# Performance work log

Measured on AMD Instinct MI355X. Metric: run time of the kernel, lower is better.

Reference implementation:

```python
import jax, jax.numpy as jnp
import numpy as np

WIN = 16
HEADS = 4


def _window_partition(x, win):
    B, H, W, C = x.shape
    x = x.reshape(B, H // win, win, W // win, win, C)
    x = x.transpose(0, 1, 3, 2, 4, 5)
    return x.reshape(-1, win * win, C)


def _reverse_window_partition(x, win, H, W):
    N, _, C = x.shape
    x = x.reshape(-1, H // win, W // win, win, win, C)
    x = x.transpose(0, 1, 3, 2, 4, 5)
    return x.reshape(-1, H, W, C)


def setup_inputs() -> dict:
    key = jax.random.key(0)
    ks = jax.random.split(key, 7)
    B, H, W, C = 2, 256, 256, 96
    s = 0.02
    return {
        "x": jax.random.normal(ks[0], (B, H, W, C), jnp.float32),
        "qkv_w": jax.random.normal(ks[1], (C, 3 * C), jnp.float32) * s,
        "qkv_b": jax.random.normal(ks[2], (3 * C,), jnp.float32) * s,
        "pe_w": jax.random.normal(ks[3], (3, 3, 1, C), jnp.float32) * s,  # depthwise HWIO
        "pe_b": jax.random.normal(ks[4], (C,), jnp.float32) * s,
        "out_w": jax.random.normal(ks[5], (C, C), jnp.float32) * s,
        "out_b": jax.random.normal(ks[6], (C,), jnp.float32) * s,
    }


def reference(x, qkv_w, qkv_b, pe_w, pe_b, out_w, out_b):
    B, H, W, C = x.shape
    win, heads = WIN, HEADS
    hd = C // heads

    z = _window_partition(x, win)
    N, S, _ = z.shape

    qkv = z @ qkv_w + qkv_b                       # (N, S, 3C)
    # headify then chunk(3): each head's 3*hd channels split into q,k,v
    qkv = qkv.reshape(N, S, heads, 3, hd).transpose(0, 2, 3, 1, 4)  # (N, h, 3, S, hd)
    q, k, v = qkv[:, :, 0], qkv[:, :, 1], qkv[:, :, 2]

    # Locally-enhanced PE: depthwise 3x3 conv on de-headified v
    v_img = v.transpose(0, 2, 1, 3).reshape(N, win, win, C)  # NHWC
    lepe = jax.lax.conv_general_dilated(
        v_img, pe_w, (1, 1), 'SAME',
        dimension_numbers=('NHWC', 'HWIO', 'NHWC'),
        feature_group_count=C) + pe_b
    lepe = lepe.reshape(N, S, heads, hd).transpose(0, 2, 1, 3)  # (N, h, S, hd)

    # per-window SDPA (default scale 1/sqrt(hd))
    scale = 1.0 / jnp.sqrt(jnp.asarray(hd, x.dtype))
    attn = jax.nn.softmax(jnp.einsum('nhsd,nhtd->nhst', q, k) * scale, axis=-1)
    o = jnp.einsum('nhst,nhtd->nhsd', attn, v) + lepe

    o = o.transpose(0, 2, 1, 3).reshape(N, S, C)
    o = _reverse_window_partition(o, win, H, W)   # (B, H, W, C)
    return o @ out_w + out_b
```

## Files before the change

kernel.cpp:

```cpp
#include <hip/hip_runtime.h>


typedef __attribute__((ext_vector_type(8))) short bf16x8;
typedef __attribute__((ext_vector_type(4))) float f32x4;

#define MFMA(a, b, c) __builtin_amdgcn_mfma_f32_16x16x32_bf16(a, b, c, 0, 0, 0)

#if __has_builtin(__builtin_amdgcn_exp2f)
#define EXP2F(x) __builtin_amdgcn_exp2f(x)
#else
#define EXP2F(x) exp2f(x)
#endif

#define SCALE2 (0.20412414523193154f * 1.4426950408889634f)

#define OFF_WT   0u
#define OFF_B2   55296u
#define OFF_WTO  56448u
#define OFF_OB   75904u

__device__ __forceinline__ unsigned short f2bf(float f) {
    union { float f; unsigned int u; } v; v.f = f;
    unsigned int u = v.u;
    return (unsigned short)((u + 0x7FFFu + ((u >> 16) & 1u)) >> 16);
}
__device__ __forceinline__ float bf2f(unsigned short h) {
    union { unsigned int u; float f; } v; v.u = ((unsigned int)h) << 16;
    return v.f;
}
__device__ __forceinline__ unsigned int pk2bf(float a, float b) {
#if __has_builtin(__builtin_amdgcn_cvt_pk_bf16_f32)
    auto p = __builtin_amdgcn_cvt_pk_bf16_f32(a, b);
    union { decltype(p) v; unsigned int u; } cv; cv.v = p;
    return cv.u;
#else
    return (unsigned int)f2bf(a) | ((unsigned int)f2bf(b) << 16);
#endif
}
__device__ __forceinline__ float frcp(float x) {
#if __has_builtin(__builtin_amdgcn_rcpf)
    return __builtin_amdgcn_rcpf(x);
#else
    return 1.0f / x;
#endif
}

__global__ void prep_kernel(const float* __restrict__ qkv_w,
                            const float* __restrict__ qkv_b,
                            const float* __restrict__ out_w,
                            unsigned short* __restrict__ wt,
                            float* __restrict__ b2,
                            unsigned short* __restrict__ wto) {
    const int stride = gridDim.x * 256;
    int i0 = blockIdx.x * 256 + threadIdx.x;
    for (int i = i0; i < 288 * 96; i += stride) {
        const int c = i / 96, k = i % 96;
        float v = qkv_w[k * 288 + c];
        if ((c % 72) < 24) v *= SCALE2;
        wt[i] = f2bf(v);
    }
    for (int i = i0; i < 288; i += stride) {
        float v = qkv_b[i];
        if ((i % 72) < 24) v *= SCALE2;
        b2[i] = v;
    }
    for (int i = i0; i < 96 * 96; i += stride) {
        const int c = i / 96, k = i % 96;
        wto[i] = f2bf(out_w[k * 96 + c]);
    }
}

__global__ __launch_bounds__(512) __attribute__((amdgpu_waves_per_eu(4, 4)))
void fused_kernel(const float* __restrict__ x,
                  const unsigned short* __restrict__ wt,
                  const float* __restrict__ b2,
                  const float* __restrict__ pe_w,
                  const float* __restrict__ pe_b,
                  unsigned short* __restrict__ Ob) {
    __shared__ unsigned short sK[256 * 24 + 8];
    __shared__ unsigned short sVT[32 * 264];
    __shared__ unsigned short sPO[8 * 32 * 40];
    __shared__ float sPW[216];
    __shared__ float sPB[24];

    const int n = blockIdx.x, tid = threadIdx.x;
    const int w = tid >> 6, l = tid & 63;
    const int lm = l & 15, lq = l >> 4;
    const int bW = n >> 8, hy = (n >> 4) & 15, wx = n & 15;
    unsigned short* Pw = &sPO[w * 32 * 40];

    if (tid < 64) {
        ushort4 ones; ones.x = ones.y = ones.z = ones.w = (unsigned short)0x3F80;
        *(ushort4*)&sVT[24 * 264 + tid * 4] = ones;
    }

    bf16x8 zf[2][3];
#pragma unroll
    for (int t4 = 0; t4 < 2; t4++) {
        const int y = w * 2 + t4;
        const size_t grow = (size_t)((bW * 256 + hy * 16 + y) * 256 + wx * 16 + lm);
        const float* xr = x + grow * 96 + lq * 8;
#pragma unroll
        for (int ks = 0; ks < 3; ks++) {
            const float4 p0 = *(const float4*)(xr + ks * 32);
            const float4 p1 = *(const float4*)(xr + ks * 32 + 4);
            union { unsigned int u[4]; bf16x8 v; } cv;
            cv.u[0] = pk2bf(p0.x, p0.y); cv.u[1] = pk2bf(p0.z, p0.w);
            cv.u[2] = pk2bf(p1.x, p1.y); cv.u[3] = pk2bf(p1.z, p1.w);
            zf[t4][ks] = cv.v;
        }
    }

    for (int h = 0; h < 4; h++) {
        __syncthreads();

#pragma unroll
        for (int mt = 0; mt < 3; mt++) {
            bf16x8 af[3];
#pragma unroll
            for (int ks = 0; ks < 3; ks++)
                af[ks] = *(const bf16x8*)(wt + (h * 72 + mt * 16 + lm) * 96 + ks * 32 + lq * 8);
            const int r48 = mt * 16 + lq * 4;
            const float4 bias = *(const float4*)(b2 + h * 72 + r48);
#pragma unroll
            for (int t4 = 0; t4 < 2; t4++) {
                f32x4 acc = {0.f, 0.f, 0.f, 0.f};
#pragma unroll
                for (int ks = 0; ks < 3; ks++) acc = MFMA(af[ks], zf[t4][ks], acc);
                uint2 pk;
                pk.x = pk2bf(acc[0] + bias.x, acc[1] + bias.y);
                pk.y = pk2bf(acc[2] + bias.z, acc[3] + bias.w);
                const int tl = t4 * 16 + lm;
                if (r48 < 24) *(uint2*)&Pw[tl * 40 + r48] = pk;
                else          *(uint2*)&sK[(w * 32 + tl) * 24 + (r48 - 24)] = pk;
            }
        }

#pragma unroll
        for (int nv = 0; nv < 2; nv++) {
            const int ch = nv * 16 + lm;
            const int vrow = h * 72 + 48 + (ch < 24 ? ch : 23);
            bf16x8 bw[3];
#pragma unroll
            for (int ks = 0; ks < 3; ks++)
                bw[ks] = *(const bf16x8*)(wt + vrow * 96 + ks * 32 + lq * 8);
            const float bv = b2[vrow];
#pragma unroll
            for (int t4 = 0; t4 < 2; t4++) {
                f32x4 acc = {0.f, 0.f, 0.f, 0.f};
#pragma unroll
                for (int ks = 0; ks < 3; ks++) acc = MFMA(zf[t4][ks], bw[ks], acc);
                if (ch < 24) {
                    uint2 pk;
                    pk.x = pk2bf(acc[0] + bv, acc[1] + bv);
                    pk.y = pk2bf(acc[2] + bv, acc[3] + bv);
                    *(uint2*)&sVT[ch * 264 + w * 32 + t4 * 16 + lq * 4] = pk;
                }
            }
        }

        for (int i = tid; i < 216; i += 512) sPW[i] = pe_w[(i / 24) * 96 + h * 24 + (i % 24)];
        if (tid < 24) sPB[tid] = pe_b[h * 24 + tid];

        __syncthreads();

        bf16x8 qf[2];
#pragma unroll
        for (int b = 0; b < 2; b++) {
            bf16x8 qv = *(const bf16x8*)&Pw[(b * 16 + lm) * 40 + lq * 8];
            if (lq == 3) qv = (bf16x8)(short)0;
            qf[b] = qv;
        }

        f32x4 oa[2][2];
#pragma unroll
        for (int b = 0; b < 2; b++)
#pragma unroll
            for (int c = 0; c < 2; c++) oa[b][c] = (f32x4){0.f, 0.f, 0.f, 0.f};

        for (int kc = 0; kc < 8; kc++) {
            bf16x8 kfc[2];
#pragma unroll
            for (int a = 0; a < 2; a++)
                kfc[a] = *(const bf16x8*)&sK[(kc * 32 + a * 16 + lm) * 24 + lq * 8];
#pragma unroll
            for (int a = 0; a < 2; a++) {
                f32x4 s[2];
#pragma unroll
                for (int b = 0; b < 2; b++)
                    s[b] = MFMA(kfc[a], qf[b], ((f32x4){0.f, 0.f, 0.f, 0.f}));
#pragma unroll
                for (int b = 0; b < 2; b++) {
                    uint2 pk;
                    pk.x = pk2bf(EXP2F(s[b][0]), EXP2F(s[b][1]));
                    pk.y = pk2bf(EXP2F(s[b][2]), EXP2F(s[b][3]));
                    *(uint2*)&Pw[(b * 16 + lm) * 40 + a * 16 + lq * 4] = pk;
                }
            }
            bf16x8 vb[2];
#pragma unroll
            for (int c = 0; c < 2; c++)
                vb[c] = *(const bf16x8*)&sVT[(c * 16 + lm) * 264 + kc * 32 + lq * 8];
#pragma unroll
            for (int b = 0; b < 2; b++) {
                const bf16x8 pa = *(const bf16x8*)&Pw[(b * 16 + lm) * 40 + lq * 8];
#pragma unroll
                for (int c = 0; c < 2; c++) oa[b][c] = MFMA(pa, vb[c], oa[b][c]);
            }
        }

        float w9[2][9], pb2[2];
#pragma unroll
        for (int c = 0; c < 2; c++) {
            const int ch = c * 16 + lm;
            if (ch < 24) {
#pragma unroll
                for (int ta = 0; ta < 9; ta++) w9[c][ta] = sPW[ta * 24 + ch];
                pb2[c] = sPB[ch];
            }
        }
#pragma unroll
        for (int b = 0; b < 2; b++) {
            float rinv[4];
#pragma unroll
            for (int r = 0; r < 4; r++)
                rinv[r] = frcp(__shfl(oa[b][1][r], (l & 48) | 8, 64));
            const int y = w * 2 + b;
            const int x0 = lq * 4;
#pragma unroll
            for (int c = 0; c < 2; c++) {
                const int ch = c * 16 + lm;
                if (ch < 24) {
                    float lep[4] = {pb2[c], pb2[c], pb2[c], pb2[c]};
                    const unsigned short* vbase = &sVT[ch * 264];
#pragma unroll
                    for (int dy = -1; dy <= 1; dy++) {
                        const int ny = y + dy;
                        if ((unsigned)ny > 15u) continue;
                        const unsigned short* vrow = vbase + ny * 16;
                        const float wl = w9[c][(dy + 1) * 3 + 0];
                        const float wm = w9[c][(dy + 1) * 3 + 1];
                        const float wr = w9[c][(dy + 1) * 3 + 2];
#pragma unroll
                        for (int d = -1; d <= 4; d++) {
                            const int xx = x0 + d;
                            if ((unsigned)xx > 15u) continue;
                            const float v = bf2f(vrow[xx]);
                            if (d - 1 >= 0 && d - 1 <= 3) lep[d - 1] = fmaf(v, wr, lep[d - 1]);
                            if (d >= 0 && d <= 3)         lep[d]     = fmaf(v, wm, lep[d]);
                            if (d + 1 <= 3)               lep[d + 1] = fmaf(v, wl, lep[d + 1]);
                        }
                    }
#pragma unroll
                    for (int r = 0; r < 4; r++) {
                        const float val = oa[b][c][r] * rinv[r] + lep[r];
                        const size_t gtok = (size_t)n * 256 + w * 32 + b * 16 + lq * 4 + r;
                        Ob[gtok * 96 + h * 24 + ch] = f2bf(val);
                    }
                }
            }
        }
    }
}

__global__ __launch_bounds__(256) __attribute__((amdgpu_waves_per_eu(4, 4)))
void oproj_kernel(const unsigned short* __restrict__ Ob,
                  const unsigned short* __restrict__ wto,
                  const float* __restrict__ out_b,
                  float* __restrict__ out) {
    const int chunk = blockIdx.x, tid = threadIdx.x;
    const int w = tid >> 6, l = tid & 63;
    const int lm = l & 15, lq = l >> 4;
    const int n = chunk >> 1;
    const int T0 = (chunk & 1) << 7;
    const int bW = n >> 8, hy = (n >> 4) & 15, wx = n & 15;
    const int tb = T0 + w * 32;
    const size_t gb = (size_t)n * 256 + tb;

    bf16x8 aO[2][3];
#pragma unroll
    for (int b = 0; b < 2; b++)
#pragma unroll
        for (int ks = 0; ks < 3; ks++)
            aO[b][ks] = *(const bf16x8*)(Ob + (gb + b * 16 + lm) * 96 + ks * 32 + lq * 8);

    f32x4 acc[2][6];
#pragma unroll
    for (int b = 0; b < 2; b++)
#pragma unroll
        for (int nt = 0; nt < 6; nt++) acc[b][nt] = (f32x4){0.f, 0.f, 0.f, 0.f};

#pragma unroll
    for (int nt = 0; nt < 6; nt++) {
#pragma unroll
        for (int ks = 0; ks < 3; ks++) {
            const bf16x8 bw = *(const bf16x8*)(wto + (nt * 16 + lm) * 96 + ks * 32 + lq * 8);
#pragma unroll
            for (int b = 0; b < 2; b++) acc[b][nt] = MFMA(aO[b][ks], bw, acc[b][nt]);
        }
    }

#pragma unroll
    for (int nt = 0; nt < 6; nt++) {
        const float bias = out_b[nt * 16 + lm];
#pragma unroll
        for (int b = 0; b < 2; b++) {
#pragma unroll
            for (int r = 0; r < 4; r++) {
                const int t = tb + b * 16 + lq * 4 + r;
                const size_t grow =
                    (size_t)((bW * 256 + hy * 16 + (t >> 4)) * 256 + wx * 16 + (t & 15));
                out[grow * 96 + nt * 16 + lm] = acc[b][nt][r] + bias;
            }
        }
    }
}

extern "C" void kernel_launch(void* const* d_in, const int* in_sizes, int n_in,
                              void* d_out, int out_size, void* d_ws, size_t ws_size,
                              hipStream_t stream) {
    const float* x     = (const float*)d_in[0];
    const float* qkv_w = (const float*)d_in[1];
    const float* qkv_b = (const float*)d_in[2];
    const float* pe_w  = (const float*)d_in[3];
    const float* pe_b  = (const float*)d_in[4];
    const float* out_w = (const float*)d_in[5];
    const float* out_b = (const float*)d_in[6];
    float* out = (float*)d_out;

    char* ws = (char*)d_ws;
    unsigned short* wt  = (unsigned short*)(ws + OFF_WT);
    float*          b2  = (float*)(ws + OFF_B2);
    unsigned short* wto = (unsigned short*)(ws + OFF_WTO);
    unsigned short* Ob  = (unsigned short*)(ws + OFF_OB);

    prep_kernel<<<72, 256, 0, stream>>>(qkv_w, qkv_b, out_w, wt, b2, wto);
    fused_kernel<<<512, 512, 0, stream>>>(x, wt, b2, pe_w, pe_b, Ob);
    oproj_kernel<<<1024, 256, 0, stream>>>(Ob, wto, out_b, out);
}
```

Before: 182.6 us.

## Store attention output head-major padded to 32 channels for oproj K-split

The intermediate attention output moves from token-major 96 channels to a head-major layout with each head padded to 32 channels, written with explicit zeros in the pad. The output projection then runs four K=32 MFMA steps, one per head, against a re-laid-out, zero-padded weight. The fused kernel's stores become full 32-channel rows per head, which may coalesce better, and oproj's launch bounds change. The cost is a third more intermediate bytes and MFMA work spent on padding.

```diff
diff --git a/kernel.cpp b/kernel.cpp
--- a/kernel.cpp
+++ b/kernel.cpp
@@ -13,11 +13,12 @@
 #endif
 
 #define SCALE2 (0.20412414523193154f * 1.4426950408889634f)
+#define NTOK 131072
 
 #define OFF_WT   0u
 #define OFF_B2   55296u
-#define OFF_WTO  56448u
-#define OFF_OB   75904u
+#define OFF_WTO2 56448u
+#define OFF_OB   81024u
 
 __device__ __forceinline__ unsigned short f2bf(float f) {
     union { float f; unsigned int u; } v; v.f = f;
@@ -50,7 +51,7 @@
                             const float* __restrict__ out_w,
                             unsigned short* __restrict__ wt,
                             float* __restrict__ b2,
-                            unsigned short* __restrict__ wto) {
+                            unsigned short* __restrict__ wto2) {
     const int stride = gridDim.x * 256;
     int i0 = blockIdx.x * 256 + threadIdx.x;
     for (int i = i0; i < 288 * 96; i += stride) {
@@ -64,9 +65,11 @@
         if ((i % 72) < 24) v *= SCALE2;
         b2[i] = v;
     }
-    for (int i = i0; i < 96 * 96; i += stride) {
-        const int c = i / 96, k = i % 96;
-        wto[i] = f2bf(out_w[k * 96 + c]);
+    for (int i = i0; i < 4 * 96 * 32; i += stride) {
+        const int h = i / 3072, rem = i % 3072;
+        const int oc = rem / 32, icl = rem % 32;
+        float v = (icl < 24) ? out_w[(h * 24 + icl) * 96 + oc] : 0.0f;
+        wto2[i] = f2bf(v);
     }
 }
 
@@ -93,6 +96,7 @@
         ushort4 ones; ones.x = ones.y = ones.z = ones.w = (unsigned short)0x3F80;
         *(ushort4*)&sVT[24 * 264 + tid * 4] = ones;
     }
+    if (tid < 8) sK[256 * 24 + tid] = 0;
 
     bf16x8 zf[2][3];
 #pragma unroll
@@ -230,8 +234,9 @@
 #pragma unroll
             for (int c = 0; c < 2; c++) {
                 const int ch = c * 16 + lm;
+                float lep[4] = {0.f, 0.f, 0.f, 0.f};
                 if (ch < 24) {
-                    float lep[4] = {pb2[c], pb2[c], pb2[c], pb2[c]};
+                    lep[0] = lep[1] = lep[2] = lep[3] = pb2[c];
                     const unsigned short* vbase = &sVT[ch * 264];
 #pragma unroll
                     for (int dy = -1; dy <= 1; dy++) {
@@ -251,21 +256,21 @@
                             if (d + 1 <= 3)               lep[d + 1] = fmaf(v, wl, lep[d + 1]);
                         }
                     }
-#pragma unroll
-                    for (int r = 0; r < 4; r++) {
-                        const float val = oa[b][c][r] * rinv[r] + lep[r];
-                        const size_t gtok = (size_t)n * 256 + w * 32 + b * 16 + lq * 4 + r;
-                        Ob[gtok * 96 + h * 24 + ch] = f2bf(val);
-                    }
                 }
-            }
-        }
-    }
-}
-
-__global__ __launch_bounds__(256) __attribute__((amdgpu_waves_per_eu(4, 4)))
+#pragma unroll
+                for (int r = 0; r < 4; r++) {
+                    const float val = (ch < 24) ? (oa[b][c][r] * rinv[r] + lep[r]) : 0.f;
+                    const size_t gtok = (size_t)n * 256 + w * 32 + b * 16 + lq * 4 + r;
+                    Ob[((size_t)h * NTOK + gtok) * 32 + ch] = f2bf(val);
+                }
+            }
+        }
+    }
+}
+
+__global__ __launch_bounds__(256, 2)
 void oproj_kernel(const unsigned short* __restrict__ Ob,
-                  const unsigned short* __restrict__ wto,
+                  const unsigned short* __restrict__ wto2,
                   const float* __restrict__ out_b,
                   float* __restrict__ out) {
     const int chunk = blockIdx.x, tid = threadIdx.x;
@@ -277,12 +282,12 @@
     const int tb = T0 + w * 32;
     const size_t gb = (size_t)n * 256 + tb;
 
-    bf16x8 aO[2][3];
+    bf16x8 aO[2][4];
 #pragma unroll
     for (int b = 0; b < 2; b++)
 #pragma unroll
-        for (int ks = 0; ks < 3; ks++)
-            aO[b][ks] = *(const bf16x8*)(Ob + (gb + b * 16 + lm) * 96 + ks * 32 + lq * 8);
+        for (int h = 0; h < 4; h++)
+            aO[b][h] = *(const bf16x8*)(Ob + ((size_t)h * NTOK + gb + b * 16 + lm) * 32 + lq * 8);
 
     f32x4 acc[2][6];
 #pragma unroll
@@ -291,14 +296,13 @@
         for (int nt = 0; nt < 6; nt++) acc[b][nt] = (f32x4){0.f, 0.f, 0.f, 0.f};
 
 #pragma unroll
-    for (int nt = 0; nt < 6; nt++) {
-#pragma unroll
-        for (int ks = 0; ks < 3; ks++) {
-            const bf16x8 bw = *(const bf16x8*)(wto + (nt * 16 + lm) * 96 + ks * 32 + lq * 8);
-#pragma unroll
-            for (int b = 0; b < 2; b++) acc[b][nt] = MFMA(aO[b][ks], bw, acc[b][nt]);
-        }
-    }
+    for (int h = 0; h < 4; h++)
+#pragma unroll
+        for (int nt = 0; nt < 6; nt++) {
+            const bf16x8 bw = *(const bf16x8*)(wto2 + (h * 96 + nt * 16 + lm) * 32 + lq * 8);
+#pragma unroll
+            for (int b = 0; b < 2; b++) acc[b][nt] = MFMA(aO[b][h], bw, acc[b][nt]);
+        }
 
 #pragma unroll
     for (int nt = 0; nt < 6; nt++) {
@@ -329,12 +333,12 @@
     float* out = (float*)d_out;
 
     char* ws = (char*)d_ws;
-    unsigned short* wt  = (unsigned short*)(ws + OFF_WT);
-    float*          b2  = (float*)(ws + OFF_B2);
-    unsigned short* wto = (unsigned short*)(ws + OFF_WTO);
-    unsigned short* Ob  = (unsigned short*)(ws + OFF_OB);
-
-    prep_kernel<<<72, 256, 0, stream>>>(qkv_w, qkv_b, out_w, wt, b2, wto);
+    unsigned short* wt   = (unsigned short*)(ws + OFF_WT);
+    float*          b2   = (float*)(ws + OFF_B2);
+    unsigned short* wto2 = (unsigned short*)(ws + OFF_WTO2);
+    unsigned short* Ob   = (unsigned short*)(ws + OFF_OB);
+
+    prep_kernel<<<72, 256, 0, stream>>>(qkv_w, qkv_b, out_w, wt, b2, wto2);
     fused_kernel<<<512, 512, 0, stream>>>(x, wt, b2, pe_w, pe_b, Ob);
-    oproj_kernel<<<1024, 256, 0, stream>>>(Ob, wto, out_b, out);
-}
+    oproj_kernel<<<1024, 256, 0, stream>>>(Ob, wto2, out_b, out);
+}
```

Result: slower. 186.4 us (+2.1%).
